# Performance work log

Hardware: AMD Instinct MI355X
Metric: run time of the kernel (lower is better)

The kernel has to match this reference:

```python
import jax, jax.numpy as jnp
import numpy as np

N, E, H, K = 2000, 512, 8, 32
DH = E // H  # 64
CLAMP = 10000.0
LN_EPS = 1e-5


def _layernorm(x, g, b):
    mu = jnp.mean(x, axis=-1, keepdims=True)
    var = jnp.mean((x - mu) ** 2, axis=-1, keepdims=True)
    return (x - mu) * jax.lax.rsqrt(var + LN_EPS) * g + b


def setup_inputs() -> dict:
    key = jax.random.key(0)
    ks = jax.random.split(key, 16)
    s_in = 1.0 / np.sqrt(E)
    inp = {
        'x': jax.random.normal(ks[0], (N, E), jnp.float32),
        'coords9': jax.random.normal(ks[1], (N, 9), jnp.float32),
        'prompt_signal': jax.random.normal(ks[2], (E,), jnp.float32),
        # pos_encoder: Linear(3, E//4) + GELU + LayerNorm(E//4)
        'pos_w1': jax.random.normal(ks[3], (E // 4, 3), jnp.float32) * 0.5,
        'pos_b1': jax.random.normal(ks[4], (E // 4,), jnp.float32) * 0.02,
        'pos_ln_g': jnp.ones((E // 4,), jnp.float32),
        'pos_ln_b': jnp.zeros((E // 4,), jnp.float32),
        # MultiheadAttention in/out projections
        'wq': jax.random.normal(ks[5], (E, E), jnp.float32) * s_in,
        'wk': jax.random.normal(ks[6], (E, E), jnp.float32) * s_in,
        'wv': jax.random.normal(ks[7], (E, E), jnp.float32) * s_in,
        'bq': jnp.zeros((E,), jnp.float32),
        'bk': jnp.zeros((E,), jnp.float32),
        'bv': jnp.zeros((E,), jnp.float32),
        'wo': jax.random.normal(ks[8], (E, E), jnp.float32) * s_in,
        'bo': jnp.zeros((E,), jnp.float32),
    }
    return inp


def reference(x, coords9, prompt_signal, pos_w1, pos_b1, pos_ln_g, pos_ln_b,
              wq, wk, wv, bq, bk, bv, wo, bo):
    n = x.shape[0]
    # centroids of triangle faces: (N,3)
    centroids = coords9.reshape(n, 3, 3).mean(axis=1)
    # pairwise centroid distances (only relation feature that affects output)
    diff = centroids[:, None, :] - centroids[None, :, :]        # (N,N,3)
    distances = jnp.linalg.norm(diff, axis=-1)                   # (N,N)
    # positional encoding branch
    pos_enc = _layernorm(jax.nn.gelu(centroids @ pos_w1.T + pos_b1, approximate=False),
                         pos_ln_g, pos_ln_b)                     # (N,E/4)
    prompt_enhanced = x + prompt_signal[None, :]
    pos_enhanced = jnp.concatenate([prompt_enhanced[:, :3 * E // 4], pos_enc], axis=-1)  # (N,E)
    # top-k nearest neighbors mask (k smallest distances per row)
    _, topk_idx = jax.lax.top_k(-distances, K)                   # (N,K)
    attn_mask = jnp.full((n, n), -jnp.inf, jnp.float32)
    attn_mask = attn_mask.at[jnp.arange(n)[:, None], topk_idx].set(0.0)
    # multi-head attention, self q=k=v, fp32
    q = (pos_enhanced @ wq.T + bq).reshape(n, H, DH)
    k = (pos_enhanced @ wk.T + bk).reshape(n, H, DH)
    v = (pos_enhanced @ wv.T + bv).reshape(n, H, DH)
    scores = jnp.einsum('nhd,mhd->hnm', q, k) / np.sqrt(DH) + attn_mask[None]
    attn = jax.nn.softmax(scores, axis=-1)                       # (H,N,N)
    ctx = jnp.einsum('hnm,mhd->nhd', attn, v).reshape(n, E)
    out = ctx @ wo.T + bo
    # _sanitize_tensor
    out = jnp.nan_to_num(out, nan=0.0, posinf=CLAMP, neginf=-CLAMP)
    return jnp.clip(out, -CLAMP, CLAMP)
```

## Files before the change

### kernel.cpp

```cpp
#include <hip/hip_runtime.h>
#include <math.h>

#define NN_K 32
#define E_DIM 512
#define CLAMP_V 10000.0f

typedef __attribute__((ext_vector_type(8))) short short8;
typedef __attribute__((ext_vector_type(4))) float f32x4;

__device__ __forceinline__ unsigned short f2bf(float x) {
  unsigned u = __float_as_uint(x);
  unsigned r = u + 0x7fffu + ((u >> 16) & 1u);
  return (unsigned short)(r >> 16);
}
__device__ __forceinline__ float bf2f_bits(short h) {
  return __uint_as_float(((unsigned)(unsigned short)h) << 16);
}

__device__ __forceinline__ void async16(const void* g, void* l) {
  __builtin_amdgcn_global_load_lds((const __attribute__((address_space(1))) void*)g,
                                   (__attribute__((address_space(3))) void*)l, 16, 0, 0);
}

__global__ __launch_bounds__(256) void front_kernel(
    const float* __restrict__ x, const float* __restrict__ coords9,
    const float* __restrict__ prompt,
    const float* __restrict__ w1, const float* __restrict__ b1,
    const float* __restrict__ ln_g, const float* __restrict__ ln_b,
    const float* __restrict__ wq, const float* __restrict__ wk,
    const float* __restrict__ wv, const float* __restrict__ wo,
    short* __restrict__ w_bf, short* __restrict__ pos_bf,
    float* __restrict__ cent, int N)
{
  int blk = blockIdx.x;
  int t = threadIdx.x;

  if (blk < 256) {
    #pragma unroll
    for (int i = 0; i < 4; ++i) {
      int v = blk * 256 + t + i * 65536;
      int m = v >> 16;
      int e = v & 0xffff;
      const float* src = m == 0 ? wq : (m == 1 ? wk : (m == 2 ? wv : wo));
      float4 f = ((const float4*)src)[e];
      short4 h;
      h.x = (short)f2bf(f.x); h.y = (short)f2bf(f.y);
      h.z = (short)f2bf(f.z); h.w = (short)f2bf(f.w);
      ((short4*)w_bf)[v] = h;
    }
    return;
  }

  int n = blk - 256;
  size_t rb = (size_t)n * E_DIM;
  if (n >= N) {
    #pragma unroll
    for (int j = t; j < E_DIM; j += 256) pos_bf[rb + j] = 0;
    return;
  }
  __shared__ float red[4];
  float g = 0.f;
  if (t < 128) {
    const float* c9 = coords9 + n * 9;
    float c0 = (c9[0] + c9[3] + c9[6]) / 3.0f;
    float c1 = (c9[1] + c9[4] + c9[7]) / 3.0f;
    float c2 = (c9[2] + c9[5] + c9[8]) / 3.0f;
    if (t == 0) {
      float4 c; c.x = c0; c.y = c1; c.z = c2; c.w = 0.f;
      ((float4*)cent)[n] = c;
    }
    float pre = c0 * w1[t*3+0] + c1 * w1[t*3+1] + c2 * w1[t*3+2] + b1[t];
    g = 0.5f * pre * (1.0f + erff(pre * 0.70710678118654752440f));
    float s = g;
    #pragma unroll
    for (int o = 32; o > 0; o >>= 1) s += __shfl_xor(s, o);
    if ((t & 63) == 0) red[t >> 6] = s;
  }
  __syncthreads();
  float mu = (red[0] + red[1]) * (1.0f / 128.0f);
  float d = g - mu;
  if (t < 128) {
    float s2 = d * d;
    #pragma unroll
    for (int o = 32; o > 0; o >>= 1) s2 += __shfl_xor(s2, o);
    if ((t & 63) == 0) red[2 + (t >> 6)] = s2;
  }
  __syncthreads();
  if (t < 128) {
    float var = (red[2] + red[3]) * (1.0f / 128.0f);
    float y = d * rsqrtf(var + 1e-5f) * ln_g[t] + ln_b[t];
    pos_bf[rb + 384 + t] = (short)f2bf(y);
  }
  #pragma unroll
  for (int j = t; j < 384; j += 256)
    pos_bf[rb + j] = (short)f2bf(x[rb + j] + prompt[j]);
}

__device__ __forceinline__ void gemm_core(
    char* smem,
    const short* __restrict__ A, const short* __restrict__ W,
    const float* __restrict__ bias,
    float* __restrict__ outf, short* __restrict__ outb,
    int out_ld, int out_c0,
    int M, int row0, int col0, bool doClamp)
{
  short* sA = (short*)smem;
  short* sB = (short*)(smem + 8192);
  int tid = threadIdx.x;
  int cr = tid >> 2;
  int ck = (tid & 3) << 3;
  const short* gA = A + (size_t)(row0 + cr) * 512 + ck;
  const short* gB = W + (size_t)(col0 + cr) * 512 + ck;
  int lo = tid * 8, loB1 = (tid + 256) * 8;
  const size_t rstep = (size_t)64 * 512;

  int lane = tid & 63, wv_ = tid >> 6;
  int wn = wv_ << 5;
  int lr = lane & 15, lq = lane >> 4;

#define STAGE(t, b) do { \
    async16(gA + (t) * 32,         sA + (b) * 2048 + lo); \
    async16(gB + (t) * 32,         sB + (b) * 4096 + lo); \
    async16(gB + (t) * 32 + rstep, sB + (b) * 4096 + loB1); } while (0)

  STAGE(0, 0);
  STAGE(1, 1);

  f32x4 acc[4][2];
  #pragma unroll
  for (int i = 0; i < 4; ++i)
    #pragma unroll
    for (int j = 0; j < 2; ++j)
      acc[i][j] = (f32x4){0.f, 0.f, 0.f, 0.f};

  #pragma unroll
  for (int it = 0; it < 16; ++it) {
    int cur = it & 1;
    if (it == 15) asm volatile("s_waitcnt vmcnt(0)\ns_barrier" ::: "memory");
    else          asm volatile("s_waitcnt vmcnt(3)\ns_barrier" ::: "memory");

    short8 af[4], bf[2];
    #pragma unroll
    for (int i = 0; i < 4; ++i)
      af[i] = *(const short8*)&sA[cur * 2048 + ((i << 4) + lr) * 32 + (lq << 3)];
    #pragma unroll
    for (int j = 0; j < 2; ++j)
      bf[j] = *(const short8*)&sB[cur * 4096 + (wn + (j << 4) + lr) * 32 + (lq << 3)];
    #pragma unroll
    for (int i = 0; i < 4; ++i)
      #pragma unroll
      for (int j = 0; j < 2; ++j)
        acc[i][j] = __builtin_amdgcn_mfma_f32_16x16x32_bf16(af[i], bf[j], acc[i][j], 0, 0, 0);

    asm volatile("s_waitcnt lgkmcnt(0)\ns_barrier" ::: "memory");
    if (it + 2 < 16) STAGE(it + 2, cur);
  }
#undef STAGE

  #pragma unroll
  for (int j = 0; j < 2; ++j) {
    int gcol = col0 + wn + (j << 4) + lr;
    float bv_ = bias[gcol];
    #pragma unroll
    for (int i = 0; i < 4; ++i) {
      #pragma unroll
      for (int r = 0; r < 4; ++r) {
        int grow = row0 + (i << 4) + (lq << 2) + r;
        if (grow < M) {
          float v = acc[i][j][r] + bv_;
          if (doClamp) {
            v = isnan(v) ? 0.0f : v;
            v = fminf(fmaxf(v, -CLAMP_V), CLAMP_V);
          }
          if (outf) outf[(size_t)grow * 512 + gcol] = v;
          else      outb[(size_t)grow * out_ld + out_c0 + gcol] = (short)f2bf(v);
        }
      }
    }
  }
}

__global__ __launch_bounds__(256) void qkv_topk(
    const short* __restrict__ A, const short* __restrict__ Wb,
    const float* __restrict__ bq, const float* __restrict__ bk, const float* __restrict__ bv,
    float* __restrict__ qb, short* __restrict__ kv,
    const float* __restrict__ cent, int* __restrict__ topk,
    int M, int N)
{
  __shared__ __align__(16) char smem[24576];
  __shared__ unsigned hist[256];
  __shared__ unsigned waveSums[4];
  __shared__ unsigned sel_bin, sel_rem;
  __shared__ unsigned cnt, tcnt;

  int by = blockIdx.y;
  if (by < 12) {
    int sel = by >> 2;
    int nblk = by & 3;
    int r0 = blockIdx.x * 64, c0 = nblk * 128;
    if (sel == 0)
      gemm_core(smem, A, Wb, bq, qb, nullptr, 512, 0, M, r0, c0, false);
    else if (sel == 1)
      gemm_core(smem, A, Wb + 262144, bk, nullptr, kv, 1024, 0, M, r0, c0, false);
    else
      gemm_core(smem, A, Wb + 2 * 262144, bv, nullptr, kv, 1024, 512, M, r0, c0, false);
    return;
  }

  int n = (by - 12) * gridDim.x + blockIdx.x;
  if (n >= N) return;
  unsigned* tie = (unsigned*)smem;

  int t = threadIdx.x;
  int lane = t & 63, wid = t >> 6;
  const float4* cq = (const float4*)cent;
  float4 c = cq[n];
  float cx = c.x, cy = c.y, cz = c.z;

  unsigned bits[8];
  #pragma unroll
  for (int r = 0; r < 8; ++r) {
    int m = t + (r << 8);
    unsigned b = 0xFFFFFFFFu;
    if (m < N) {
      float4 cm = cq[m];
      float dx = cx - cm.x, dy = cy - cm.y, dz = cz - cm.z;
      float dist = sqrtf(dx*dx + dy*dy + dz*dz);
      b = __float_as_uint(dist);
    }
    bits[r] = b;
  }

  unsigned prefix = 0;
  unsigned K_rem = NN_K;
  #pragma unroll
  for (int p = 0; p < 4; ++p) {
    int shift = 24 - 8 * p;
    unsigned high_mask = (p == 0) ? 0u : (0xFFFFFFFFu << (8 * (4 - p)));
    hist[t] = 0;
    __syncthreads();
    #pragma unroll
    for (int r = 0; r < 8; ++r) {
      if ((bits[r] & high_mask) == prefix)
        atomicAdd(&hist[(bits[r] >> shift) & 255], 1u);
    }
    __syncthreads();
    unsigned h = hist[t];
    unsigned scan = h;
    #pragma unroll
    for (int o = 1; o < 64; o <<= 1) {
      unsigned u = __shfl_up(scan, o);
      if (lane >= o) scan += u;
    }
    if (lane == 63) waveSums[wid] = scan;
    __syncthreads();
    unsigned off = 0;
    for (int w = 0; w < wid; ++w) off += waveSums[w];
    scan += off;
    if (scan >= K_rem && (scan - h) < K_rem) {
      sel_bin = (unsigned)t;
      sel_rem = K_rem - (scan - h);
    }
    __syncthreads();
    prefix |= sel_bin << shift;
    K_rem = sel_rem;
    __syncthreads();
  }

  unsigned T = prefix;
  if (t == 0) { cnt = 0; tcnt = 0; }
  __syncthreads();
  #pragma unroll
  for (int r = 0; r < 8; ++r) {
    int m = t + (r << 8);
    if (m < N) {
      if (bits[r] < T) {
        unsigned slot = atomicAdd(&cnt, 1u);
        topk[n * NN_K + slot] = m;
      } else if (bits[r] == T) {
        unsigned tp = atomicAdd(&tcnt, 1u);
        tie[tp] = (unsigned)m;
      }
    }
  }
  __syncthreads();
  if (t == 0) {
    unsigned base = cnt;
    unsigned need = K_rem;
    for (unsigned it = 0; it < need; ++it) {
      unsigned best = 0xFFFFFFFFu, bj = 0;
      for (unsigned j = 0; j < tcnt; ++j)
        if (tie[j] < best) { best = tie[j]; bj = j; }
      topk[n * NN_K + base + it] = (int)best;
      tie[bj] = 0xFFFFFFFFu;
    }
  }
}

__global__ __launch_bounds__(256) void out_mfma(
    const short* __restrict__ A, const short* __restrict__ Wb,
    const float* __restrict__ bias, float* __restrict__ out, int M)
{
  __shared__ __align__(16) char smem[24576];
  gemm_core(smem, A, Wb + (size_t)3 * 262144, bias, out, nullptr, 512, 0, M,
            blockIdx.x * 64, blockIdx.y * 128, true);
}

__global__ __launch_bounds__(512) void attn_kernel(
    const float* __restrict__ qb, const short* __restrict__ kv,
    const int* __restrict__ topk, short* __restrict__ ctx_bf, int N)
{
  __shared__ short klds[32 * 512];
  __shared__ int sidx[NN_K];
  __shared__ float plds[8 * 32];

  int n = blockIdx.x;
  int tid = threadIdx.x;
  size_t rb = (size_t)n * E_DIM;
  if (n >= N) { ctx_bf[rb + tid] = 0; return; }

  if (tid < NN_K) sidx[tid] = topk[n * NN_K + tid];
  __syncthreads();

  int h = tid >> 6, lane = tid & 63;
  int jk = lane & 31, half = lane >> 5;
  int dbase = h * 64 + half * 32;

  float qv[32];
  {
    const float4* qs = (const float4*)(qb + rb + dbase);
    #pragma unroll
    for (int b = 0; b < 8; ++b) {
      float4 f = qs[b];
      qv[b*4+0] = f.x; qv[b*4+1] = f.y; qv[b*4+2] = f.z; qv[b*4+3] = f.w;
    }
  }

  {
    int j = tid >> 4, a = tid & 15;
    const short8* src = (const short8*)(kv + (size_t)sidx[j] * 1024 + a * 32);
    int sw = 4 * (j & 15);
    short* row = &klds[j * 512];
    #pragma unroll
    for (int b = 0; b < 4; ++b) {
      short8 val = src[b];
      int d0 = a * 32 + b * 8;
      *(short4*)&row[(d0    ) ^ sw] = *(const short4*)&val;
      *(short4*)&row[(d0 + 4) ^ sw] = *((const short4*)&val + 1);
    }
  }
  __syncthreads();

  float s = 0.f;
  {
    int sw = 4 * (jk & 15);
    const short* krow = &klds[jk * 512];
    #pragma unroll
    for (int i4 = 0; i4 < 8; ++i4) {
      short4 kkv = *(const short4*)&krow[(dbase + i4 * 4) ^ sw];
      s += qv[i4*4+0] * bf2f_bits(kkv.x) + qv[i4*4+1] * bf2f_bits(kkv.y)
         + qv[i4*4+2] * bf2f_bits(kkv.z) + qv[i4*4+3] * bf2f_bits(kkv.w);
    }
  }
  s += __shfl_xor(s, 32);
  s *= 0.125f;

  float mx = s;
  #pragma unroll
  for (int o = 16; o > 0; o >>= 1) mx = fmaxf(mx, __shfl_xor(mx, o));
  float p = expf(s - mx);
  float l = p;
  #pragma unroll
  for (int o = 16; o > 0; o >>= 1) l += __shfl_xor(l, o);
  p *= (1.0f / l);
  if (half == 0) plds[h * 32 + jk] = p;
  __syncthreads();

  float pv[32];
  #pragma unroll
  for (int b = 0; b < 8; ++b) {
    float4 f = *(const float4*)&plds[h * 32 + b * 4];
    pv[b*4+0] = f.x; pv[b*4+1] = f.y; pv[b*4+2] = f.z; pv[b*4+3] = f.w;
  }

  int off = 512 + h * 64 + lane;
  float acc = 0.f;
  #pragma unroll
  for (int j = 0; j < NN_K; ++j)
    acc += pv[j] * bf2f_bits(kv[(size_t)sidx[j] * 1024 + off]);
  ctx_bf[rb + h * 64 + lane] = (short)f2bf(acc);
}

extern "C" void kernel_launch(void* const* d_in, const int* in_sizes, int n_in,
                              void* d_out, int out_size, void* d_ws, size_t ws_size,
                              hipStream_t stream) {
  const float* x       = (const float*)d_in[0];
  const float* coords9 = (const float*)d_in[1];
  const float* prompt  = (const float*)d_in[2];
  const float* pos_w1  = (const float*)d_in[3];
  const float* pos_b1  = (const float*)d_in[4];
  const float* ln_g    = (const float*)d_in[5];
  const float* ln_b    = (const float*)d_in[6];
  const float* wq      = (const float*)d_in[7];
  const float* wk      = (const float*)d_in[8];
  const float* wv      = (const float*)d_in[9];
  const float* bq      = (const float*)d_in[10];
  const float* bk      = (const float*)d_in[11];
  const float* bv      = (const float*)d_in[12];
  const float* wo      = (const float*)d_in[13];
  const float* bo      = (const float*)d_in[14];

  int N = in_sizes[1] / 9;
  int Mpad = (N + 127) & ~127;
  size_t PE = (size_t)Mpad * E_DIM;

  char* p = (char*)d_ws;
  short* pos_bf = (short*)p; p += PE * 2;
  short* w_bf   = (short*)p; p += (size_t)4 * 512 * 512 * 2;
  float* qb     = (float*)p; p += PE * 4;
  short* kv_bf  = (short*)p; p += PE * 2 * 2;
  short* ctx_bf = (short*)p; p += PE * 2;
  int*   topk   = (int*)p;   p += (size_t)Mpad * NN_K * 4;
  float* cent   = (float*)p;

  front_kernel<<<256 + Mpad, 256, 0, stream>>>(
      x, coords9, prompt, pos_w1, pos_b1, ln_g, ln_b,
      wq, wk, wv, wo, w_bf, pos_bf, cent, N);

  int gx = Mpad / 64;
  dim3 gq(gx, 12 + (N + gx - 1) / gx);
  qkv_topk<<<gq, 256, 0, stream>>>(pos_bf, w_bf, bq, bk, bv, qb, kv_bf,
                                   cent, topk, Mpad, N);
  attn_kernel<<<Mpad, 512, 0, stream>>>(qb, kv_bf, topk, ctx_bf, N);

  dim3 go(Mpad / 64, 4);
  out_mfma<<<go, 256, 0, stream>>>(ctx_bf, w_bf, bo, (float*)d_out, N);
}
```

Before: 154.7 us.

## Replace four-pass radix top-k select with single 12-bit histogram pass plus rank sort

The top-k neighbor selection now builds one 4096-bin histogram of the top 12 bits of the distance, kept as per-wave packed 16-bit counters in shared memory, instead of four 8-bit radix passes that each need several barriers. Candidates that fall in the boundary bin are gathered into a tie buffer and ranked in parallel by one wave using (distance, index) comparisons, replacing the serial single-thread minimum search. This cuts barriers and serial work per row. In exchange the boundary bin can hold many candidates, making the quadratic rank step costly, and the buffer is capped at 1024 entries, so overflow would give wrong results.

```diff
diff --git a/kernel.cpp b/kernel.cpp
--- a/kernel.cpp
+++ b/kernel.cpp
@@ -188,9 +188,8 @@
     int M, int N)
 {
   __shared__ __align__(16) char smem[24576];
-  __shared__ unsigned hist[256];
   __shared__ unsigned waveSums[4];
-  __shared__ unsigned sel_bin, sel_rem;
+  __shared__ unsigned selB, selNeed;
   __shared__ unsigned cnt, tcnt;
 
   int by = blockIdx.y;
@@ -209,13 +208,19 @@
 
   int n = (by - 12) * gridDim.x + blockIdx.x;
   if (n >= N) return;
-  unsigned* tie = (unsigned*)smem;
+
+  unsigned* wh   = (unsigned*)smem;
+  unsigned* tieB = (unsigned*)(smem + 16384);
+  unsigned* tieI = (unsigned*)(smem + 20480);
 
   int t = threadIdx.x;
   int lane = t & 63, wid = t >> 6;
   const float4* cq = (const float4*)cent;
   float4 c = cq[n];
   float cx = c.x, cy = c.y, cz = c.z;
+
+  #pragma unroll
+  for (int i = 0; i < 16; ++i) wh[t + i * 256] = 0;
 
   unsigned bits[8];
   #pragma unroll
@@ -230,69 +235,79 @@
     }
     bits[r] = b;
   }
-
-  unsigned prefix = 0;
-  unsigned K_rem = NN_K;
-  #pragma unroll
-  for (int p = 0; p < 4; ++p) {
-    int shift = 24 - 8 * p;
-    unsigned high_mask = (p == 0) ? 0u : (0xFFFFFFFFu << (8 * (4 - p)));
-    hist[t] = 0;
-    __syncthreads();
-    #pragma unroll
-    for (int r = 0; r < 8; ++r) {
-      if ((bits[r] & high_mask) == prefix)
-        atomicAdd(&hist[(bits[r] >> shift) & 255], 1u);
-    }
-    __syncthreads();
-    unsigned h = hist[t];
-    unsigned scan = h;
-    #pragma unroll
-    for (int o = 1; o < 64; o <<= 1) {
-      unsigned u = __shfl_up(scan, o);
-      if (lane >= o) scan += u;
-    }
-    if (lane == 63) waveSums[wid] = scan;
-    __syncthreads();
-    unsigned off = 0;
-    for (int w = 0; w < wid; ++w) off += waveSums[w];
-    scan += off;
-    if (scan >= K_rem && (scan - h) < K_rem) {
-      sel_bin = (unsigned)t;
-      sel_rem = K_rem - (scan - h);
-    }
-    __syncthreads();
-    prefix |= sel_bin << shift;
-    K_rem = sel_rem;
-    __syncthreads();
-  }
-
-  unsigned T = prefix;
+  __syncthreads();
+
+  unsigned* myh = wh + (wid << 10);
+  #pragma unroll
+  for (int r = 0; r < 8; ++r) {
+    if (bits[r] != 0xFFFFFFFFu) {
+      unsigned bin = bits[r] >> 20;
+      atomicAdd(&myh[bin >> 1], 1u << ((bin & 1) << 4));
+    }
+  }
+  __syncthreads();
+
+  unsigned bc[8];
+  unsigned tot = 0;
+  #pragma unroll
+  for (int w = 0; w < 4; ++w) {
+    int iw = (t << 2) + w;
+    unsigned s = wh[iw] + wh[1024 + iw] + wh[2048 + iw] + wh[3072 + iw];
+    bc[w * 2]     = s & 0xFFFFu;
+    bc[w * 2 + 1] = s >> 16;
+    tot += (s & 0xFFFFu) + (s >> 16);
+  }
+  unsigned scan = tot;
+  #pragma unroll
+  for (int o = 1; o < 64; o <<= 1) {
+    unsigned u = __shfl_up(scan, o);
+    if (lane >= o) scan += u;
+  }
+  if (lane == 63) waveSums[wid] = scan;
+  __syncthreads();
+  unsigned off = 0;
+  for (int w = 0; w < wid; ++w) off += waveSums[w];
+  unsigned incl = scan + off;
+  unsigned excl = incl - tot;
+  if (excl < NN_K && incl >= NN_K) {
+    unsigned cacc = excl;
+    #pragma unroll
+    for (int b = 0; b < 8; ++b) {
+      if (cacc + bc[b] >= NN_K) { selB = (unsigned)(t * 8 + b); selNeed = NN_K - cacc; break; }
+      cacc += bc[b];
+    }
+  }
   if (t == 0) { cnt = 0; tcnt = 0; }
   __syncthreads();
+
+  unsigned B = selB;
   #pragma unroll
   for (int r = 0; r < 8; ++r) {
-    int m = t + (r << 8);
-    if (m < N) {
-      if (bits[r] < T) {
+    if (bits[r] != 0xFFFFFFFFu) {
+      unsigned bin = bits[r] >> 20;
+      if (bin < B) {
         unsigned slot = atomicAdd(&cnt, 1u);
-        topk[n * NN_K + slot] = m;
-      } else if (bits[r] == T) {
+        topk[n * NN_K + slot] = t + (r << 8);
+      } else if (bin == B) {
         unsigned tp = atomicAdd(&tcnt, 1u);
-        tie[tp] = (unsigned)m;
+        if (tp < 1024u) { tieB[tp] = bits[r]; tieI[tp] = (unsigned)(t + (r << 8)); }
       }
     }
   }
   __syncthreads();
-  if (t == 0) {
+
+  if (t < 64) {
     unsigned base = cnt;
-    unsigned need = K_rem;
-    for (unsigned it = 0; it < need; ++it) {
-      unsigned best = 0xFFFFFFFFu, bj = 0;
-      for (unsigned j = 0; j < tcnt; ++j)
-        if (tie[j] < best) { best = tie[j]; bj = j; }
-      topk[n * NN_K + base + it] = (int)best;
-      tie[bj] = 0xFFFFFFFFu;
+    unsigned need = selNeed;
+    unsigned tn = tcnt > 1024u ? 1024u : tcnt;
+    for (unsigned j = lane; j < tn; j += 64) {
+      unsigned kb = tieB[j], ki = tieI[j];
+      unsigned rank = 0;
+      for (unsigned i = 0; i < tn; ++i) {
+        unsigned ib = tieB[i];
+        rank += (ib < kb) || (ib == kb && tieI[i] < ki);
+      }
+      if (rank < need) topk[n * NN_K + base + rank] = (int)ki;
     }
   }
 }
```

After: 138.7 us. -10.4%, faster.
